# Optimization experiments

Hardware: AMD Instinct MI355X
Metric: run time of the kernel (lower is better)

Reference implementation:

```python
import jax, jax.numpy as jnp
import numpy as np

B, N, F, H = 8, 2048, 64, 1

def setup_inputs() -> dict:
    key = jax.random.key(0)
    k1, k2, k3, k4 = jax.random.split(key, 4)
    return {
        "encode": jax.random.normal(k1, (B, N, F), dtype=jnp.float32),
        "kernel": jax.random.normal(k2, (F, H, F), dtype=jnp.float32) * 0.1,
        "attn_kernel_self": jax.random.normal(k3, (F, H, 1), dtype=jnp.float32) * 0.1,
        "attn_kernel_neighs": jax.random.normal(k4, (F, H, 1), dtype=jnp.float32) * 0.1,
    }

def reference(encode, kernel, attn_kernel_self, attn_kernel_neighs):
    # project: [B,N,F] x [F,H,F] -> [B,N,H,F]
    h = jnp.einsum('bni,iho->bnho', encode, kernel)
    # per-node scalar scores: [B,N,H,1]
    a_self = jnp.einsum('bnhi,iho->bnho', h, attn_kernel_self)
    a_neigh = jnp.einsum('bnhi,iho->bnho', h, attn_kernel_neighs)
    # transpose last three axes (...ABC -> ...CBA): [B,1,H,N]
    a_neigh_t = jnp.transpose(a_neigh, (0, 3, 2, 1))
    # broadcast-sum -> [B,N,H,N] dense logits, leaky_relu(alpha=0.2), softmax over neighbors
    logits = jax.nn.leaky_relu(a_self + a_neigh_t, negative_slope=0.2)
    coef = jax.nn.softmax(logits, axis=-1)
    # mean over heads (axis=2) -> [B,N,N]
    return jnp.mean(coef, axis=2)
```

## Files before the change

kernel.cpp:

```cpp
#include <hip/hip_runtime.h>

#define BB 8
#define NN 2048
#define FF 64
#define LOG2E 1.4426950408889634f
#define ROWS_PER_WAVE 4

typedef float f32x4 __attribute__((ext_vector_type(4)));

__global__ __launch_bounds__(256) void scores_fused(const float* __restrict__ enc,
                                                    const float* __restrict__ kmat,
                                                    const float* __restrict__ aks,
                                                    const float* __restrict__ akn,
                                                    float* __restrict__ S,
                                                    float* __restrict__ T) {
    __shared__ float ws[FF], wn[FF];
    const int tid = threadIdx.x;
    if (tid < FF) {
        float s = 0.f, t = 0.f;
        #pragma unroll
        for (int o = 0; o < FF; ++o) {
            float k = kmat[tid * FF + o];
            s += k * aks[o];
            t += k * akn[o];
        }
        ws[tid] = s;
        wn[tid] = t;
    }
    __syncthreads();

    const int g = blockIdx.x * 256 + tid;
    const f32x4* e4 = (const f32x4*)(enc + (size_t)g * FF);
    const f32x4* w4 = (const f32x4*)ws;
    const f32x4* v4 = (const f32x4*)wn;
    float s = 0.f, t = 0.f;
    #pragma unroll
    for (int j = 0; j < FF / 4; ++j) {
        f32x4 e = e4[j];
        f32x4 w = w4[j];
        f32x4 v = v4[j];
        s += e.x * w.x + e.y * w.y + e.z * w.z + e.w * w.w;
        t += e.x * v.x + e.y * v.y + e.z * v.z + e.w * v.w;
    }
    S[g] = s * LOG2E;
    T[g] = t * LOG2E;
}

__device__ __forceinline__ float waveMax(float v) {
    #pragma unroll
    for (int o = 32; o > 0; o >>= 1) v = fmaxf(v, __shfl_xor(v, o, 64));
    return v;
}
__device__ __forceinline__ float waveSum(float v) {
    #pragma unroll
    for (int o = 32; o > 0; o >>= 1) v += __shfl_xor(v, o, 64);
    return v;
}
__device__ __forceinline__ float lk(float x) { return fmaxf(x, 0.2f * x); }

__global__ __launch_bounds__(256) void softmax_kernel(const float* __restrict__ S,
                                                      const float* __restrict__ T,
                                                      float* __restrict__ out) {
    const int wave = threadIdx.x >> 6;
    const int lane = threadIdx.x & 63;
    const int row0 = (blockIdx.x * 4 + wave) * ROWS_PER_WAVE;
    const int b    = row0 >> 11;

    const f32x4* t4 = (const f32x4*)(T + (size_t)b * NN);

    f32x4 t[8];
    float tm = -3.4e38f;
    #pragma unroll
    for (int j = 0; j < 8; ++j) {
        t[j] = t4[lane + 64 * j];
        tm = fmaxf(tm, fmaxf(fmaxf(t[j].x, t[j].y), fmaxf(t[j].z, t[j].w)));
    }
    const float tmax = waveMax(tm);

    f32x4 E[8], F[8];
    #pragma unroll
    for (int j = 0; j < 8; ++j) {
        f32x4 d;
        d.x = t[j].x - tmax; d.y = t[j].y - tmax;
        d.z = t[j].z - tmax; d.w = t[j].w - tmax;
        E[j].x = __builtin_exp2f(d.x); E[j].y = __builtin_exp2f(d.y);
        E[j].z = __builtin_exp2f(d.z); E[j].w = __builtin_exp2f(d.w);
        F[j].x = __builtin_exp2f(0.2f * d.x); F[j].y = __builtin_exp2f(0.2f * d.y);
        F[j].z = __builtin_exp2f(0.2f * d.z); F[j].w = __builtin_exp2f(0.2f * d.w);
    }

    #pragma unroll
    for (int r = 0; r < ROWS_PER_WAVE; ++r) {
        const int row = row0 + r;
        const float s = S[row];
        const float u = s + tmax;
        const float M = lk(u);
        const float A  = __builtin_exp2f(u - M);
        const float Bc = __builtin_exp2f(0.2f * u - M);

        f32x4 e[8];
        float ls = 0.f;
        #pragma unroll
        for (int j = 0; j < 8; ++j) {
            e[j].x = fmaxf(A * E[j].x, Bc * F[j].x);
            e[j].y = fmaxf(A * E[j].y, Bc * F[j].y);
            e[j].z = fmaxf(A * E[j].z, Bc * F[j].z);
            e[j].w = fmaxf(A * E[j].w, Bc * F[j].w);
            ls += (e[j].x + e[j].y) + (e[j].z + e[j].w);
        }
        ls = waveSum(ls);
        const float inv = 1.f / ls;

        f32x4* o4 = (f32x4*)(out + (size_t)row * NN);
        #pragma unroll
        for (int j = 0; j < 8; ++j) {
            f32x4 o;
            o.x = e[j].x * inv; o.y = e[j].y * inv;
            o.z = e[j].z * inv; o.w = e[j].w * inv;
            __builtin_nontemporal_store(o, &o4[lane + 64 * j]);
        }
    }
}

extern "C" void kernel_launch(void* const* d_in, const int* in_sizes, int n_in,
                              void* d_out, int out_size, void* d_ws, size_t ws_size,
                              hipStream_t stream) {
    const float* enc  = (const float*)d_in[0];
    const float* kmat = (const float*)d_in[1];
    const float* aks  = (const float*)d_in[2];
    const float* akn  = (const float*)d_in[3];
    float* out = (float*)d_out;

    float* W = (float*)d_ws;
    float* S = W;
    float* T = W + BB * NN;

    scores_fused<<<BB * NN / 256, 256, 0, stream>>>(enc, kmat, aks, akn, S, T);
    softmax_kernel<<<BB * NN / (4 * ROWS_PER_WAVE), 256, 0, stream>>>(S, T, out);
}
```

Before: 34.25 us.

## Fuse score projection and softmax into one kernel with per-block T recompute

```diff
diff --git a/kernel.cpp b/kernel.cpp
--- a/kernel.cpp
+++ b/kernel.cpp
@@ -4,18 +4,37 @@
 #define NN 2048
 #define FF 64
 #define LOG2E 1.4426950408889634f
-#define ROWS_PER_WAVE 4
+#define ROWS_PER_BLOCK 32
 
 typedef float f32x4 __attribute__((ext_vector_type(4)));
 
-__global__ __launch_bounds__(256) void scores_fused(const float* __restrict__ enc,
-                                                    const float* __restrict__ kmat,
-                                                    const float* __restrict__ aks,
-                                                    const float* __restrict__ akn,
-                                                    float* __restrict__ S,
-                                                    float* __restrict__ T) {
+__device__ __forceinline__ float waveMax(float v) {
+    #pragma unroll
+    for (int o = 32; o > 0; o >>= 1) v = fmaxf(v, __shfl_xor(v, o, 64));
+    return v;
+}
+__device__ __forceinline__ float waveSum(float v) {
+    #pragma unroll
+    for (int o = 32; o > 0; o >>= 1) v += __shfl_xor(v, o, 64);
+    return v;
+}
+__device__ __forceinline__ float lk(float x) { return fmaxf(x, 0.2f * x); }
+
+__global__ __launch_bounds__(256) void gat_fused(const float* __restrict__ enc,
+                                                 const float* __restrict__ kmat,
+                                                 const float* __restrict__ aks,
+                                                 const float* __restrict__ akn,
+                                                 float* __restrict__ out) {
     __shared__ float ws[FF], wn[FF];
-    const int tid = threadIdx.x;
+    __shared__ float Tld[NN];
+    __shared__ float sS[ROWS_PER_BLOCK];
+    __shared__ float wred[4];
+
+    const int tid  = threadIdx.x;
+    const int wave = tid >> 6, lane = tid & 63;
+    const int row0 = blockIdx.x * ROWS_PER_BLOCK;
+    const int b    = row0 >> 11;
+
     if (tid < FF) {
         float s = 0.f, t = 0.f;
         #pragma unroll
@@ -29,45 +48,33 @@
     }
     __syncthreads();
 
-    const int g = blockIdx.x * 256 + tid;
-    const f32x4* e4 = (const f32x4*)(enc + (size_t)g * FF);
+    const float* encb = enc + (size_t)b * NN * FF;
+    const f32x4* v4 = (const f32x4*)wn;
     const f32x4* w4 = (const f32x4*)ws;
-    const f32x4* v4 = (const f32x4*)wn;
-    float s = 0.f, t = 0.f;
     #pragma unroll
-    for (int j = 0; j < FF / 4; ++j) {
-        f32x4 e = e4[j];
-        f32x4 w = w4[j];
-        f32x4 v = v4[j];
-        s += e.x * w.x + e.y * w.y + e.z * w.z + e.w * w.w;
-        t += e.x * v.x + e.y * v.y + e.z * v.z + e.w * v.w;
+    for (int m = tid; m < NN; m += 256) {
+        const f32x4* e4 = (const f32x4*)(encb + (size_t)m * FF);
+        float t = 0.f;
+        #pragma unroll
+        for (int j = 0; j < FF / 4; ++j) {
+            f32x4 e = e4[j], v = v4[j];
+            t += e.x * v.x + e.y * v.y + e.z * v.z + e.w * v.w;
+        }
+        Tld[m] = t * LOG2E;
     }
-    S[g] = s * LOG2E;
-    T[g] = t * LOG2E;
-}
+    if (tid < ROWS_PER_BLOCK) {
+        const f32x4* e4 = (const f32x4*)(enc + (size_t)(row0 + tid) * FF);
+        float s = 0.f;
+        #pragma unroll
+        for (int j = 0; j < FF / 4; ++j) {
+            f32x4 e = e4[j], w = w4[j];
+            s += e.x * w.x + e.y * w.y + e.z * w.z + e.w * w.w;
+        }
+        sS[tid] = s * LOG2E;
+    }
+    __syncthreads();
 
-__device__ __forceinline__ float waveMax(float v) {
-    #pragma unroll
-    for (int o = 32; o > 0; o >>= 1) v = fmaxf(v, __shfl_xor(v, o, 64));
-    return v;
-}
-__device__ __forceinline__ float waveSum(float v) {
-    #pragma unroll
-    for (int o = 32; o > 0; o >>= 1) v += __shfl_xor(v, o, 64);
-    return v;
-}
-__device__ __forceinline__ float lk(float x) { return fmaxf(x, 0.2f * x); }
-
-__global__ __launch_bounds__(256) void softmax_kernel(const float* __restrict__ S,
-                                                      const float* __restrict__ T,
-                                                      float* __restrict__ out) {
-    const int wave = threadIdx.x >> 6;
-    const int lane = threadIdx.x & 63;
-    const int row0 = (blockIdx.x * 4 + wave) * ROWS_PER_WAVE;
-    const int b    = row0 >> 11;
-
-    const f32x4* t4 = (const f32x4*)(T + (size_t)b * NN);
-
+    const f32x4* t4 = (const f32x4*)Tld;
     f32x4 t[8];
     float tm = -3.4e38f;
     #pragma unroll
@@ -75,7 +82,10 @@
         t[j] = t4[lane + 64 * j];
         tm = fmaxf(tm, fmaxf(fmaxf(t[j].x, t[j].y), fmaxf(t[j].z, t[j].w)));
     }
-    const float tmax = waveMax(tm);
+    tm = waveMax(tm);
+    if (lane == 0) wred[wave] = tm;
+    __syncthreads();
+    const float tmax = fmaxf(fmaxf(wred[0], wred[1]), fmaxf(wred[2], wred[3]));
 
     f32x4 E[8], F[8];
     #pragma unroll
@@ -90,9 +100,9 @@
     }
 
     #pragma unroll
-    for (int r = 0; r < ROWS_PER_WAVE; ++r) {
-        const int row = row0 + r;
-        const float s = S[row];
+    for (int k = 0; k < 8; ++k) {
+        const int r = wave + 4 * k;
+        const float s = sS[r];
         const float u = s + tmax;
         const float M = lk(u);
         const float A  = __builtin_exp2f(u - M);
@@ -111,7 +121,7 @@
         ls = waveSum(ls);
         const float inv = 1.f / ls;
 
-        f32x4* o4 = (f32x4*)(out + (size_t)row * NN);
+        f32x4* o4 = (f32x4*)(out + (size_t)(row0 + r) * NN);
         #pragma unroll
         for (int j = 0; j < 8; ++j) {
             f32x4 o;
@@ -131,10 +141,5 @@
     const float* akn  = (const float*)d_in[3];
     float* out = (float*)d_out;
 
-    float* W = (float*)d_ws;
-    float* S = W;
-    float* T = W + BB * NN;
-
-    scores_fused<<<BB * NN / 256, 256, 0, stream>>>(enc, kmat, aks, akn, S, T);
-    softmax_kernel<<<BB * NN / (4 * ROWS_PER_WAVE), 256, 0, stream>>>(S, T, out);
+    gat_fused<<<BB * NN / ROWS_PER_BLOCK, 256, 0, stream>>>(enc, kmat, aks, akn, out);
 }
```

Result: slower. 57.88 us (+69.0%).
